# Kernel tuning notes

Measured on AMD Instinct MI355X. Metric: run time of the kernel, lower is better.

The kernel has to match this reference:

```python
import jax, jax.numpy as jnp
import numpy as np

NUM_HEADS = 16
EPS = 1e-5
CHUNK = 128  # chunk length for the chunked recurrent-state scan


def _linear_attention(x, Wq, Wk, Wv, Wo, bo):
    B, T, E = x.shape
    H = NUM_HEADS
    d = E // H

    def proj(W):
        # nn.Linear(bias=False): y = x @ W.T ; split heads -> (B,H,T,d)
        return (x @ W.T).reshape(B, T, H, d).transpose(0, 2, 1, 3)

    phi_q = jax.nn.elu(proj(Wq)) + 1.0
    phi_k = jax.nn.elu(proj(Wk)) + 1.0
    V = proj(Wv)

    nC = T // CHUNK
    # (nC, B, H, C, d) so lax.scan iterates over chunks of time
    def to_chunks(a):
        return a.reshape(B, H, nC, CHUNK, d).transpose(2, 0, 1, 3, 4)

    qc, kc, vc = to_chunks(phi_q), to_chunks(phi_k), to_chunks(V)
    mask = jnp.tril(jnp.ones((CHUNK, CHUNK), x.dtype))  # causal incl. diagonal

    S0 = jnp.zeros((B, H, d, d), x.dtype)  # running sum of k v^T
    z0 = jnp.zeros((B, H, d), x.dtype)     # running sum of phi_k

    def step(carry, inp):
        S, z = carry
        q, k, v = inp  # (B,H,C,d)
        A = jnp.einsum('bhid,bhjd->bhij', q, k) * mask
        num = jnp.einsum('bhij,bhjd->bhid', A, v) + jnp.einsum('bhid,bhde->bhie', q, S)
        den = jnp.sum(A, axis=-1) + jnp.einsum('bhid,bhd->bhi', q, z) + EPS
        out = num / den[..., None]
        S = S + jnp.einsum('bhjd,bhje->bhde', k, v)
        z = z + jnp.sum(k, axis=2)
        return (S, z), out

    _, outs = jax.lax.scan(step, (S0, z0), (qc, kc, vc))  # (nC,B,H,C,d)
    out = outs.transpose(1, 2, 0, 3, 4).reshape(B, H, T, d)
    out = out.transpose(0, 2, 1, 3).reshape(B, T, E)
    # out_proj (dropout p=0 / eval -> identity)
    return out @ Wo.T + bo


def setup_inputs() -> dict:
    key = jax.random.key(0)
    ks = jax.random.split(key, 6)
    B, T, E = 2, 2048, 1024
    s = 1.0 / np.sqrt(E)
    return {
        'x': jax.random.normal(ks[0], (B, T, E), jnp.float32),
        'Wq': jax.random.normal(ks[1], (E, E), jnp.float32) * s,
        'Wk': jax.random.normal(ks[2], (E, E), jnp.float32) * s,
        'Wv': jax.random.normal(ks[3], (E, E), jnp.float32) * s,
        'Wo': jax.random.normal(ks[4], (E, E), jnp.float32) * s,
        'bo': jnp.zeros((E,), jnp.float32),
    }


def reference(x, Wq, Wk, Wv, Wo, bo):
    return _linear_attention(x, Wq, Wk, Wv, Wo, bo)
```

## Files before the change

kernel.cpp:

```cpp
#include <hip/hip_runtime.h>
#include <hip/hip_bf16.h>
#include <stdint.h>

typedef __attribute__((ext_vector_type(4))) float  floatx4;
typedef __attribute__((ext_vector_type(8))) short  short8;
typedef __attribute__((ext_vector_type(8))) unsigned short ushortx8;
typedef __attribute__((ext_vector_type(4))) unsigned short ushortx4;

#define B_  2
#define T_  2048
#define E_  1024
#define H_  16
#define D_  64
#define C_  128
#define NC_ 16
#define M_  4096
#define EPS_ 1e-5f

__device__ __forceinline__ unsigned short f2b(float f) {
    union { float f; unsigned int u; } v; v.f = f;
    unsigned int r = v.u + 0x7fffu + ((v.u >> 16) & 1u);
    return (unsigned short)(r >> 16);
}
__device__ __forceinline__ float b2f(unsigned short b) {
    union { unsigned int u; float f; } v; v.u = ((unsigned int)b) << 16;
    return v.f;
}

__device__ __forceinline__ int stage_seg(int i) { return (i & 3) ^ ((i >> 3) & 3); }
__device__ __forceinline__ int frag_slot(int lane) {
    int m = lane & 15, q = lane >> 4;
    return m * 4 + (q ^ ((m >> 1) & 3));
}

__global__ __launch_bounds__(256) void convert_kernel(const float* __restrict__ src,
                                                      unsigned short* __restrict__ dst, int n) {
    int i = (blockIdx.x * 256 + threadIdx.x) * 4;
    if (i < n) {
        float4 f = *(const float4*)(src + i);
        ushortx4 o;
        o[0] = f2b(f.x); o[1] = f2b(f.y); o[2] = f2b(f.z); o[3] = f2b(f.w);
        *(ushortx4*)(dst + i) = o;
    }
}

__global__ __launch_bounds__(256) void gemm_qkv(const unsigned short* __restrict__ A,
                                                const unsigned short* __restrict__ Bm,
                                                unsigned short* __restrict__ Cb) {
    const int N = 3 * E_, K = E_;
    __shared__ __align__(16) unsigned short at[8 * 512];
    __shared__ __align__(16) unsigned short bt[8 * 512];
    int tid = threadIdx.x;
    int wave = tid >> 6, lane = tid & 63;
    int wr = wave >> 1, wc = wave & 1;
    int m = lane & 15, q = lane >> 4;
    int srow = lane >> 2, sseg = stage_seg(lane);
    int fs = frag_slot(lane);
    int row0 = blockIdx.y * 128, col0 = blockIdx.x * 128;
    floatx4 acc[4][4];
    for (int i = 0; i < 4; i++) for (int j = 0; j < 4; j++) acc[i][j] = floatx4{0.f, 0.f, 0.f, 0.f};

    for (int k0 = 0; k0 < K; k0 += 32) {
        __syncthreads();
        for (int p = 0; p < 2; p++) {
            int t = p * 4 + wave;
            const unsigned short* ga = A  + (size_t)(row0 + t * 16 + srow) * K + k0 + sseg * 8;
            const unsigned short* gb = Bm + (size_t)(col0 + t * 16 + srow) * K + k0 + sseg * 8;
            __builtin_amdgcn_global_load_lds((const __attribute__((address_space(1))) unsigned int*)ga,
                (__attribute__((address_space(3))) unsigned int*)(at + t * 512), 16, 0, 0);
            __builtin_amdgcn_global_load_lds((const __attribute__((address_space(1))) unsigned int*)gb,
                (__attribute__((address_space(3))) unsigned int*)(bt + t * 512), 16, 0, 0);
        }
        __syncthreads();
        short8 af[4], bfr[4];
        for (int mi = 0; mi < 4; mi++) af[mi]  = *(const short8*)(at + (wr * 4 + mi) * 512 + fs * 8);
        for (int ni = 0; ni < 4; ni++) bfr[ni] = *(const short8*)(bt + (wc * 4 + ni) * 512 + fs * 8);
        for (int mi = 0; mi < 4; mi++)
            for (int ni = 0; ni < 4; ni++)
                acc[mi][ni] = __builtin_amdgcn_mfma_f32_16x16x32_bf16(af[mi], bfr[ni], acc[mi][ni], 0, 0, 0);
    }
    int qrow = q * 4;
    for (int mi = 0; mi < 4; mi++) for (int ni = 0; ni < 4; ni++) {
        int col = col0 + wc * 64 + ni * 16 + m;
        bool isphi = (col < 2 * E_);
        for (int r2 = 0; r2 < 4; r2++) {
            int row = row0 + wr * 64 + mi * 16 + qrow + r2;
            float v = acc[mi][ni][r2];
            if (isphi) v = (v > 0.f) ? (v + 1.f) : __expf(v);
            Cb[(size_t)row * N + col] = f2b(v);
        }
    }
}

__global__ __launch_bounds__(256) void gemm_out(const unsigned short* __restrict__ A,
                                                const unsigned short* __restrict__ Bm,
                                                const float* __restrict__ bias,
                                                float* __restrict__ Cf) {
    const int N = E_, K = E_;
    __shared__ __align__(16) unsigned short at[4 * 512];
    __shared__ __align__(16) unsigned short bt[8 * 512];
    int tid = threadIdx.x;
    int wave = tid >> 6, lane = tid & 63;
    int m = lane & 15, q = lane >> 4;
    int srow = lane >> 2, sseg = stage_seg(lane);
    int fs = frag_slot(lane);
    int row0 = blockIdx.y * 64, col0 = blockIdx.x * 128;
    floatx4 acc[4][2];
    for (int i = 0; i < 4; i++) for (int j = 0; j < 2; j++) acc[i][j] = floatx4{0.f, 0.f, 0.f, 0.f};

    for (int k0 = 0; k0 < K; k0 += 32) {
        __syncthreads();
        {
            const unsigned short* ga  = A  + (size_t)(row0 + wave * 16 + srow) * K + k0 + sseg * 8;
            __builtin_amdgcn_global_load_lds((const __attribute__((address_space(1))) unsigned int*)ga,
                (__attribute__((address_space(3))) unsigned int*)(at + wave * 512), 16, 0, 0);
            for (int p = 0; p < 2; p++) {
                int t = wave * 2 + p;
                const unsigned short* gb = Bm + (size_t)(col0 + t * 16 + srow) * K + k0 + sseg * 8;
                __builtin_amdgcn_global_load_lds((const __attribute__((address_space(1))) unsigned int*)gb,
                    (__attribute__((address_space(3))) unsigned int*)(bt + t * 512), 16, 0, 0);
            }
        }
        __syncthreads();
        short8 af[4], bfr[2];
        for (int mi = 0; mi < 4; mi++) af[mi]  = *(const short8*)(at + mi * 512 + fs * 8);
        for (int ci = 0; ci < 2; ci++) bfr[ci] = *(const short8*)(bt + (wave * 2 + ci) * 512 + fs * 8);
        for (int mi = 0; mi < 4; mi++)
            for (int ci = 0; ci < 2; ci++)
                acc[mi][ci] = __builtin_amdgcn_mfma_f32_16x16x32_bf16(af[mi], bfr[ci], acc[mi][ci], 0, 0, 0);
    }
    int qrow = q * 4;
    for (int ci = 0; ci < 2; ci++) {
        int col = col0 + wave * 32 + ci * 16 + m;
        float bv = bias[col];
        for (int mi = 0; mi < 4; mi++)
            for (int r2 = 0; r2 < 4; r2++) {
                int row = row0 + mi * 16 + qrow + r2;
                Cf[(size_t)row * N + col] = acc[mi][ci][r2] + bv;
            }
    }
}

__global__ __launch_bounds__(256) void chunk_sums(const unsigned short* __restrict__ qkv,
                                                  float* __restrict__ Sc, float* __restrict__ zc) {
    int c = blockIdx.x, h = blockIdx.y, bb = blockIdx.z;
    __shared__ __align__(16) unsigned short Kt[64 * 132];
    __shared__ __align__(16) unsigned short Vt[80 * 132];
    int tid = threadIdx.x;
    int lane = tid & 63, w = tid >> 6;
    size_t rowb = (size_t)bb * T_ + (size_t)c * C_;
    int kcol = E_ + h * D_, vcol = 2 * E_ + h * D_;

    for (int s = 0; s < 4; s++) {
        int off = s * 256 + tid;
        int r = off >> 3, seg = (off & 7) * 8;
        size_t g = (rowb + r) * 3072;
        ushortx8 k8 = *(const ushortx8*)(qkv + g + kcol + seg);
        ushortx8 v8 = *(const ushortx8*)(qkv + g + vcol + seg);
        for (int e = 0; e < 8; e++) {
            Kt[(seg + e) * 132 + r] = k8[e];
            Vt[(seg + e) * 132 + r] = v8[e];
        }
    }
    if (tid < 128) Vt[64 * 132 + tid] = 0x3f80;
    __syncthreads();

    floatx4 acc[5];
    for (int ni = 0; ni < 5; ni++) acc[ni] = floatx4{0.f, 0.f, 0.f, 0.f};
    int lm = lane & 15, lk = (lane >> 4) * 8;
    for (int k0 = 0; k0 < 128; k0 += 32) {
        short8 af = *(const short8*)(Kt + (w * 16 + lm) * 132 + k0 + lk);
        for (int ni = 0; ni < 5; ni++) {
            short8 bf = *(const short8*)(Vt + (ni * 16 + lm) * 132 + k0 + lk);
            acc[ni] = __builtin_amdgcn_mfma_f32_16x16x32_bf16(af, bf, acc[ni], 0, 0, 0);
        }
    }
    size_t base = ((size_t)(bb * H_ + h) * NC_ + c) * (size_t)(D_ * D_);
    int r0 = w * 16 + (lane >> 4) * 4;
    for (int ni = 0; ni < 4; ni++)
        for (int reg = 0; reg < 4; reg++)
            Sc[base + (size_t)(r0 + reg) * D_ + ni * 16 + lm] = acc[ni][reg];
    if (lm == 0) {
        size_t zb = ((size_t)(bb * H_ + h) * NC_ + c) * D_;
        for (int reg = 0; reg < 4; reg++) zc[zb + r0 + reg] = acc[4][reg];
    }
}

__global__ __launch_bounds__(256) void attn_kernel(const unsigned short* __restrict__ qkv,
                                                   const float* __restrict__ Sc,
                                                   const float* __restrict__ zc,
                                                   unsigned short* __restrict__ attn) {
    int c = blockIdx.x, h = blockIdx.y, bb = blockIdx.z;
    __shared__ __align__(16) unsigned short qs[128 * 68];
    __shared__ __align__(16) unsigned short ks[128 * 68];
    __shared__ __align__(16) unsigned short vt[64 * 132];
    __shared__ __align__(16) unsigned short ovl[128 * 36];
    __shared__ float zsh[64];
    int tid = threadIdx.x;
    int lane = tid & 63, w = tid >> 6;
    int lm = lane & 15, lq = lane >> 4;
    size_t rowb = (size_t)bb * T_ + (size_t)c * C_;
    int qcol = h * D_, kcol = E_ + h * D_, vcol = 2 * E_ + h * D_;

    for (int s = 0; s < 4; s++) {
        int off = s * 256 + tid;
        int r = off >> 3, seg = (off & 7) * 8;
        size_t g = (rowb + r) * 3072;
        ushortx8 q8 = *(const ushortx8*)(qkv + g + qcol + seg);
        ushortx8 k8 = *(const ushortx8*)(qkv + g + kcol + seg);
        ushortx8 v8 = *(const ushortx8*)(qkv + g + vcol + seg);
        *(ushortx8*)(qs + r * 68 + seg) = q8;
        *(ushortx8*)(ks + r * 68 + seg) = k8;
        for (int e = 0; e < 8; e++) vt[(seg + e) * 132 + r] = v8[e];
    }
    {
        size_t scb = ((size_t)(bb * H_ + h) * NC_) * (size_t)(D_ * D_);
        int p = tid * 16;
        float a[16];
        for (int i = 0; i < 16; i++) a[i] = 0.f;
        for (int j = 0; j < c; j++) {
            const float* Sj = Sc + scb + (size_t)j * (D_ * D_) + p;
            for (int q = 0; q < 16; q += 4) {
                float4 f = *(const float4*)(Sj + q);
                a[q] += f.x; a[q + 1] += f.y; a[q + 2] += f.z; a[q + 3] += f.w;
            }
        }
        for (int i = 0; i < 16; i++) {
            int d = (p + i) >> 6, e = (p + i) & 63;
            ovl[e * 68 + d] = f2b(a[i]);
        }
    }
    if (tid < 64) {
        size_t zb = ((size_t)(bb * H_ + h) * NC_) * D_;
        float zr = 0.f;
        for (int j = 0; j < c; j++) zr += zc[zb + (size_t)j * D_ + tid];
        zsh[tid] = zr;
    }
    __syncthreads();

    floatx4 acc[2][4];
    for (int mi = 0; mi < 2; mi++) for (int ni = 0; ni < 4; ni++) acc[mi][ni] = floatx4{0.f, 0.f, 0.f, 0.f};
    for (int k0 = 0; k0 < 64; k0 += 32) {
        short8 aq[2];
        for (int mi = 0; mi < 2; mi++)
            aq[mi] = *(const short8*)(qs + (w * 32 + mi * 16 + lm) * 68 + k0 + lq * 8);
        for (int ni = 0; ni < 4; ni++) {
            short8 bs = *(const short8*)(ovl + (ni * 16 + lm) * 68 + k0 + lq * 8);
            for (int mi = 0; mi < 2; mi++)
                acc[mi][ni] = __builtin_amdgcn_mfma_f32_16x16x32_bf16(aq[mi], bs, acc[mi][ni], 0, 0, 0);
        }
    }
    float dsum[2][4];
    {
        int d0 = lm * 4;
        float4 z4 = *(const float4*)(zsh + d0);
        for (int mi = 0; mi < 2; mi++)
            for (int reg = 0; reg < 4; reg++) {
                int row = w * 32 + mi * 16 + lq * 4 + reg;
                ushortx4 q4 = *(const ushortx4*)(qs + row * 68 + d0);
                dsum[mi][reg] = b2f(q4[0]) * z4.x + b2f(q4[1]) * z4.y + b2f(q4[2]) * z4.z + b2f(q4[3]) * z4.w;
            }
    }
    __syncthreads();

    for (int jt = 0; jt <= w; jt++) {
        floatx4 pa[2][2];
        for (int mi = 0; mi < 2; mi++) for (int ct = 0; ct < 2; ct++) pa[mi][ct] = floatx4{0.f, 0.f, 0.f, 0.f};
        for (int k0 = 0; k0 < 64; k0 += 32) {
            short8 aq[2];
            for (int mi = 0; mi < 2; mi++)
                aq[mi] = *(const short8*)(qs + (w * 32 + mi * 16 + lm) * 68 + k0 + lq * 8);
            for (int ct = 0; ct < 2; ct++) {
                short8 bk = *(const short8*)(ks + (jt * 32 + ct * 16 + lm) * 68 + k0 + lq * 8);
                for (int mi = 0; mi < 2; mi++)
                    pa[mi][ct] = __builtin_amdgcn_mfma_f32_16x16x32_bf16(aq[mi], bk, pa[mi][ct], 0, 0, 0);
            }
        }
        bool diag = (jt == w);
        for (int mi = 0; mi < 2; mi++)
            for (int ct = 0; ct < 2; ct++)
                for (int reg = 0; reg < 4; reg++) {
                    int il = mi * 16 + lq * 4 + reg;
                    int jl = ct * 16 + lm;
                    float v = pa[mi][ct][reg];
                    if (diag && jl > il) v = 0.f;
                    dsum[mi][reg] += v;
                    ovl[(w * 32 + il) * 36 + jl] = f2b(v);
                }
        short8 ap[2];
        for (int mi = 0; mi < 2; mi++)
            ap[mi] = *(const short8*)(ovl + (w * 32 + mi * 16 + lm) * 36 + lq * 8);
        for (int ni = 0; ni < 4; ni++) {
            short8 bv = *(const short8*)(vt + (ni * 16 + lm) * 132 + jt * 32 + lq * 8);
            for (int mi = 0; mi < 2; mi++)
                acc[mi][ni] = __builtin_amdgcn_mfma_f32_16x16x32_bf16(ap[mi], bv, acc[mi][ni], 0, 0, 0);
        }
    }

    for (int off = 1; off < 16; off <<= 1)
        for (int mi = 0; mi < 2; mi++)
            for (int reg = 0; reg < 4; reg++)
                dsum[mi][reg] += __shfl_xor(dsum[mi][reg], off);

    for (int mi = 0; mi < 2; mi++)
        for (int reg = 0; reg < 4; reg++) {
            float inv = 1.f / (dsum[mi][reg] + EPS_);
            int row = w * 32 + mi * 16 + lq * 4 + reg;
            for (int ni = 0; ni < 4; ni++)
                attn[(rowb + row) * E_ + h * D_ + ni * 16 + lm] = f2b(acc[mi][ni][reg] * inv);
        }
}

extern "C" void kernel_launch(void* const* d_in, const int* in_sizes, int n_in,
                              void* d_out, int out_size, void* d_ws, size_t ws_size,
                              hipStream_t stream) {
    const float* x  = (const float*)d_in[0];
    const float* Wq = (const float*)d_in[1];
    const float* Wk = (const float*)d_in[2];
    const float* Wv = (const float*)d_in[3];
    const float* Wo = (const float*)d_in[4];
    const float* bo = (const float*)d_in[5];
    float* out = (float*)d_out;

    const size_t MB = 1024 * 1024;
    uint8_t* ws = (uint8_t*)d_ws;
    unsigned short* xb    = (unsigned short*)(ws + 0);
    unsigned short* wb    = (unsigned short*)(ws + 8 * MB);
    unsigned short* wob   = (unsigned short*)(ws + 14 * MB);
    unsigned short* qkvb  = (unsigned short*)(ws + 16 * MB);
    float* Sc = (float*)(ws + 40 * MB);
    float* zc = (float*)(ws + 48 * MB);
    unsigned short* attnb = xb;

    convert_kernel<<<(M_ * E_) / 1024, 256, 0, stream>>>(x, xb, M_ * E_);
    convert_kernel<<<(E_ * E_) / 1024, 256, 0, stream>>>(Wq, wb,              E_ * E_);
    convert_kernel<<<(E_ * E_) / 1024, 256, 0, stream>>>(Wk, wb + E_ * E_,    E_ * E_);
    convert_kernel<<<(E_ * E_) / 1024, 256, 0, stream>>>(Wv, wb + 2 * E_ * E_, E_ * E_);
    convert_kernel<<<(E_ * E_) / 1024, 256, 0, stream>>>(Wo, wob, E_ * E_);

    gemm_qkv<<<dim3(24, 32), 256, 0, stream>>>(xb, wb, qkvb);
    chunk_sums<<<dim3(NC_, H_, B_), 256, 0, stream>>>(qkvb, Sc, zc);
    attn_kernel<<<dim3(NC_, H_, B_), 256, 0, stream>>>(qkvb, Sc, zc, attnb);
    gemm_out<<<dim3(8, 64), 256, 0, stream>>>(attnb, wob, bo, out);
}
```

Measured before the change: 188.0 us.

## Double K-tile depth in GEMMs and merge weight conversions into one launch

```diff
diff --git a/kernel.cpp b/kernel.cpp
--- a/kernel.cpp
+++ b/kernel.cpp
@@ -44,12 +44,27 @@
     }
 }
 
+__global__ __launch_bounds__(256) void convert4_kernel(const float* __restrict__ s0,
+                                                       const float* __restrict__ s1,
+                                                       const float* __restrict__ s2,
+                                                       const float* __restrict__ s3,
+                                                       unsigned short* __restrict__ dst) {
+    int i = (blockIdx.x * 256 + threadIdx.x) * 4;
+    int which = i >> 20;
+    const float* s = (which == 0) ? s0 : (which == 1) ? s1 : (which == 2) ? s2 : s3;
+    int off = i & ((1 << 20) - 1);
+    float4 f = *(const float4*)(s + off);
+    ushortx4 o;
+    o[0] = f2b(f.x); o[1] = f2b(f.y); o[2] = f2b(f.z); o[3] = f2b(f.w);
+    *(ushortx4*)(dst + i) = o;
+}
+
 __global__ __launch_bounds__(256) void gemm_qkv(const unsigned short* __restrict__ A,
                                                 const unsigned short* __restrict__ Bm,
                                                 unsigned short* __restrict__ Cb) {
     const int N = 3 * E_, K = E_;
-    __shared__ __align__(16) unsigned short at[8 * 512];
-    __shared__ __align__(16) unsigned short bt[8 * 512];
+    __shared__ __align__(16) unsigned short at[16 * 512];
+    __shared__ __align__(16) unsigned short bt[16 * 512];
     int tid = threadIdx.x;
     int wave = tid >> 6, lane = tid & 63;
     int wr = wave >> 1, wc = wave & 1;
@@ -60,24 +75,27 @@
     floatx4 acc[4][4];
     for (int i = 0; i < 4; i++) for (int j = 0; j < 4; j++) acc[i][j] = floatx4{0.f, 0.f, 0.f, 0.f};
 
-    for (int k0 = 0; k0 < K; k0 += 32) {
+    for (int k0 = 0; k0 < K; k0 += 64) {
         __syncthreads();
-        for (int p = 0; p < 2; p++) {
+        for (int p = 0; p < 4; p++) {
             int t = p * 4 + wave;
-            const unsigned short* ga = A  + (size_t)(row0 + t * 16 + srow) * K + k0 + sseg * 8;
-            const unsigned short* gb = Bm + (size_t)(col0 + t * 16 + srow) * K + k0 + sseg * 8;
+            int rt = t & 7, kh = t >> 3;
+            const unsigned short* ga = A  + (size_t)(row0 + rt * 16 + srow) * K + k0 + kh * 32 + sseg * 8;
+            const unsigned short* gb = Bm + (size_t)(col0 + rt * 16 + srow) * K + k0 + kh * 32 + sseg * 8;
             __builtin_amdgcn_global_load_lds((const __attribute__((address_space(1))) unsigned int*)ga,
                 (__attribute__((address_space(3))) unsigned int*)(at + t * 512), 16, 0, 0);
             __builtin_amdgcn_global_load_lds((const __attribute__((address_space(1))) unsigned int*)gb,
                 (__attribute__((address_space(3))) unsigned int*)(bt + t * 512), 16, 0, 0);
         }
         __syncthreads();
-        short8 af[4], bfr[4];
-        for (int mi = 0; mi < 4; mi++) af[mi]  = *(const short8*)(at + (wr * 4 + mi) * 512 + fs * 8);
-        for (int ni = 0; ni < 4; ni++) bfr[ni] = *(const short8*)(bt + (wc * 4 + ni) * 512 + fs * 8);
-        for (int mi = 0; mi < 4; mi++)
-            for (int ni = 0; ni < 4; ni++)
-                acc[mi][ni] = __builtin_amdgcn_mfma_f32_16x16x32_bf16(af[mi], bfr[ni], acc[mi][ni], 0, 0, 0);
+        for (int kh = 0; kh < 2; kh++) {
+            short8 af[4], bfr[4];
+            for (int mi = 0; mi < 4; mi++) af[mi]  = *(const short8*)(at + (kh * 8 + wr * 4 + mi) * 512 + fs * 8);
+            for (int ni = 0; ni < 4; ni++) bfr[ni] = *(const short8*)(bt + (kh * 8 + wc * 4 + ni) * 512 + fs * 8);
+            for (int mi = 0; mi < 4; mi++)
+                for (int ni = 0; ni < 4; ni++)
+                    acc[mi][ni] = __builtin_amdgcn_mfma_f32_16x16x32_bf16(af[mi], bfr[ni], acc[mi][ni], 0, 0, 0);
+        }
     }
     int qrow = q * 4;
     for (int mi = 0; mi < 4; mi++) for (int ni = 0; ni < 4; ni++) {
@@ -97,8 +115,8 @@
                                                 const float* __restrict__ bias,
                                                 float* __restrict__ Cf) {
     const int N = E_, K = E_;
-    __shared__ __align__(16) unsigned short at[4 * 512];
-    __shared__ __align__(16) unsigned short bt[8 * 512];
+    __shared__ __align__(16) unsigned short at[8 * 512];
+    __shared__ __align__(16) unsigned short bt[16 * 512];
     int tid = threadIdx.x;
     int wave = tid >> 6, lane = tid & 63;
     int m = lane & 15, q = lane >> 4;
@@ -108,26 +126,31 @@
     floatx4 acc[4][2];
     for (int i = 0; i < 4; i++) for (int j = 0; j < 2; j++) acc[i][j] = floatx4{0.f, 0.f, 0.f, 0.f};
 
-    for (int k0 = 0; k0 < K; k0 += 32) {
+    for (int k0 = 0; k0 < K; k0 += 64) {
         __syncthreads();
-        {
-            const unsigned short* ga  = A  + (size_t)(row0 + wave * 16 + srow) * K + k0 + sseg * 8;
+        for (int p = 0; p < 2; p++) {
+            int ta = p * 4 + wave;
+            int rta = ta & 3, kha = ta >> 2;
+            const unsigned short* ga = A + (size_t)(row0 + rta * 16 + srow) * K + k0 + kha * 32 + sseg * 8;
             __builtin_amdgcn_global_load_lds((const __attribute__((address_space(1))) unsigned int*)ga,
-                (__attribute__((address_space(3))) unsigned int*)(at + wave * 512), 16, 0, 0);
-            for (int p = 0; p < 2; p++) {
-                int t = wave * 2 + p;
-                const unsigned short* gb = Bm + (size_t)(col0 + t * 16 + srow) * K + k0 + sseg * 8;
-                __builtin_amdgcn_global_load_lds((const __attribute__((address_space(1))) unsigned int*)gb,
-                    (__attribute__((address_space(3))) unsigned int*)(bt + t * 512), 16, 0, 0);
-            }
+                (__attribute__((address_space(3))) unsigned int*)(at + ta * 512), 16, 0, 0);
+        }
+        for (int p = 0; p < 4; p++) {
+            int tb = p * 4 + wave;
+            int rtb = tb & 7, khb = tb >> 3;
+            const unsigned short* gb = Bm + (size_t)(col0 + rtb * 16 + srow) * K + k0 + khb * 32 + sseg * 8;
+            __builtin_amdgcn_global_load_lds((const __attribute__((address_space(1))) unsigned int*)gb,
+                (__attribute__((address_space(3))) unsigned int*)(bt + tb * 512), 16, 0, 0);
         }
         __syncthreads();
-        short8 af[4], bfr[2];
-        for (int mi = 0; mi < 4; mi++) af[mi]  = *(const short8*)(at + mi * 512 + fs * 8);
-        for (int ci = 0; ci < 2; ci++) bfr[ci] = *(const short8*)(bt + (wave * 2 + ci) * 512 + fs * 8);
-        for (int mi = 0; mi < 4; mi++)
-            for (int ci = 0; ci < 2; ci++)
-                acc[mi][ci] = __builtin_amdgcn_mfma_f32_16x16x32_bf16(af[mi], bfr[ci], acc[mi][ci], 0, 0, 0);
+        for (int kh = 0; kh < 2; kh++) {
+            short8 af[4], bfr[2];
+            for (int mi = 0; mi < 4; mi++) af[mi]  = *(const short8*)(at + (kh * 4 + mi) * 512 + fs * 8);
+            for (int ci = 0; ci < 2; ci++) bfr[ci] = *(const short8*)(bt + (kh * 8 + wave * 2 + ci) * 512 + fs * 8);
+            for (int mi = 0; mi < 4; mi++)
+                for (int ci = 0; ci < 2; ci++)
+                    acc[mi][ci] = __builtin_amdgcn_mfma_f32_16x16x32_bf16(af[mi], bfr[ci], acc[mi][ci], 0, 0, 0);
+        }
     }
     int qrow = q * 4;
     for (int ci = 0; ci < 2; ci++) {
@@ -326,17 +349,14 @@
     uint8_t* ws = (uint8_t*)d_ws;
     unsigned short* xb    = (unsigned short*)(ws + 0);
     unsigned short* wb    = (unsigned short*)(ws + 8 * MB);
-    unsigned short* wob   = (unsigned short*)(ws + 14 * MB);
+    unsigned short* wob   = wb + 3 * E_ * E_;
     unsigned short* qkvb  = (unsigned short*)(ws + 16 * MB);
     float* Sc = (float*)(ws + 40 * MB);
     float* zc = (float*)(ws + 48 * MB);
     unsigned short* attnb = xb;
 
     convert_kernel<<<(M_ * E_) / 1024, 256, 0, stream>>>(x, xb, M_ * E_);
-    convert_kernel<<<(E_ * E_) / 1024, 256, 0, stream>>>(Wq, wb,              E_ * E_);
-    convert_kernel<<<(E_ * E_) / 1024, 256, 0, stream>>>(Wk, wb + E_ * E_,    E_ * E_);
-    convert_kernel<<<(E_ * E_) / 1024, 256, 0, stream>>>(Wv, wb + 2 * E_ * E_, E_ * E_);
-    convert_kernel<<<(E_ * E_) / 1024, 256, 0, stream>>>(Wo, wob, E_ * E_);
+    convert4_kernel<<<(4 * E_ * E_) / 1024, 256, 0, stream>>>(Wq, Wk, Wv, Wo, wb);
 
     gemm_qkv<<<dim3(24, 32), 256, 0, stream>>>(xb, wb, qkvb);
     chunk_sums<<<dim3(NC_, H_, B_), 256, 0, stream>>>(qkvb, Sc, zc);
```

After: 174.9 us. 7.0% less time.
